# Optimization experiments

Measured on AMD Instinct MI355X. Metric: run time of the kernel, lower is better.

## Reference

```python
import jax, jax.numpy as jnp
import numpy as np
import math

HIDDEN = 256
HEADS = 8
HEAD_DIM = HIDDEN // HEADS
SCALE = math.sqrt(HEAD_DIM)


def setup_inputs() -> dict:
    key = jax.random.key(0)
    ks = jax.random.split(key, 10)
    B, N = 2, 4096
    x = jax.random.normal(ks[0], (B, N, HIDDEN), dtype=jnp.float32)
    pos = jax.random.normal(ks[1], (B, N, 3), dtype=jnp.float32)
    s = 1.0 / math.sqrt(HIDDEN)
    Wq = jax.random.normal(ks[2], (HIDDEN, HIDDEN), dtype=jnp.float32) * s
    bq = jnp.zeros((HIDDEN,), dtype=jnp.float32)
    Wk = jax.random.normal(ks[3], (HIDDEN, HIDDEN), dtype=jnp.float32) * s
    bk = jnp.zeros((HIDDEN,), dtype=jnp.float32)
    Wv = jax.random.normal(ks[4], (HIDDEN, HIDDEN), dtype=jnp.float32) * s
    bv = jnp.zeros((HIDDEN,), dtype=jnp.float32)
    Wo = jax.random.normal(ks[5], (HIDDEN, HIDDEN), dtype=jnp.float32) * s
    bo = jnp.zeros((HIDDEN,), dtype=jnp.float32)
    return {"x": x, "pos": pos, "Wq": Wq, "bq": bq, "Wk": Wk, "bk": bk,
            "Wv": Wv, "bv": bv, "Wo": Wo, "bo": bo}


def _pairwise_dist(pos):
    # Euclidean cdist via the norm trick; clip for numerical safety.
    sq = jnp.sum(pos * pos, axis=-1)  # [B, N]
    d2 = sq[:, :, None] + sq[:, None, :] - 2.0 * jnp.einsum('bic,bjc->bij', pos, pos)
    return jnp.sqrt(jnp.maximum(d2, 0.0))  # [B, N, N]


def reference(x, pos, Wq, bq, Wk, bk, Wv, bv, Wo, bo):
    B, N, _ = x.shape
    # projections -> [B, H, N, Dh]
    def split_heads(t):
        return t.reshape(B, N, HEADS, HEAD_DIM).transpose(0, 2, 1, 3)
    q = split_heads(x @ Wq.T + bq)
    k = split_heads(x @ Wk.T + bk)
    v = split_heads(x @ Wv.T + bv)
    scores = jnp.einsum('bhid,bhjd->bhij', q, k) / SCALE
    dist_bias = -_pairwise_dist(pos) / 10.0  # [B, N, N]
    scores = scores + dist_bias[:, None, :, :]
    attn = jax.nn.softmax(scores, axis=-1)
    out = jnp.einsum('bhij,bhjd->bhid', attn, v)
    out = out.transpose(0, 2, 1, 3).reshape(B, N, HIDDEN)
    return out @ Wo.T + bo
```

## Files before the change

kernel.cpp:

```cpp
#include <hip/hip_runtime.h>

#define BATCH 2
#define SEQ   4096
#define HID   256
#define NHEAD 8
#define DH    32
#define THR_L2 11.5f
#define QSCALE 0.25501639769925074f
#define BIASC (-0.14426950408889634f)

typedef __attribute__((ext_vector_type(8))) _Float16 half8;
typedef __attribute__((ext_vector_type(4))) _Float16 half4;
typedef __attribute__((ext_vector_type(2))) __fp16   fp16x2;
typedef __attribute__((ext_vector_type(4))) float    f32x4;

__device__ __forceinline__ float fast_exp2(float x) {
    return __builtin_amdgcn_exp2f(x);
}

__global__ void cvt_f32_f16(const float* __restrict__ src,
                            _Float16* __restrict__ dst, int n) {
    int i = (blockIdx.x * blockDim.x + threadIdx.x) * 4;
    if (i >= n) return;
    f32x4 v = *reinterpret_cast<const f32x4*>(src + i);
    half4 h;
#pragma unroll
    for (int c = 0; c < 4; ++c) h[c] = (_Float16)v[c];
    *reinterpret_cast<half4*>(dst + i) = h;
}

__global__ void cvt_w4(const float* __restrict__ a, const float* __restrict__ b,
                       const float* __restrict__ c, const float* __restrict__ d,
                       _Float16* __restrict__ dst) {
    const float* srcs[4] = {a, b, c, d};
    const float* s = srcs[blockIdx.y];
    const int i = (blockIdx.x * blockDim.x + threadIdx.x) * 4;
    f32x4 v = *reinterpret_cast<const f32x4*>(s + i);
    half4 h;
#pragma unroll
    for (int k = 0; k < 4; ++k) h[k] = (_Float16)v[k];
    *reinterpret_cast<half4*>(dst + (size_t)blockIdx.y * HID * HID + i) = h;
}

__global__ __launch_bounds__(256) void qkv_proj(
    const _Float16* __restrict__ xh, const _Float16* __restrict__ Wh,
    const float* __restrict__ bq, const float* __restrict__ bk,
    const float* __restrict__ bv,
    _Float16* __restrict__ Qh, _Float16* __restrict__ Kh,
    _Float16* __restrict__ Vt)
{
    const int z   = blockIdx.z;
    const int m0  = blockIdx.x * 64;
    const int n0  = blockIdx.y * 64;
    const int tid = threadIdx.x;
    const int w   = tid >> 6, lane = tid & 63;
    const int lr  = lane & 15, lg = lane >> 4;
    const int wr  = (w >> 1) * 32, wc = (w & 1) * 32;

    const _Float16* Wp = Wh + (size_t)z * HID * HID;
    const float* bias = (z == 0) ? bq : (z == 1) ? bk : bv;

    f32x4 acc[2][2] = {};
    const int ar = m0 + wr + lr;
    const int br = n0 + wc + lr;
#pragma unroll
    for (int ks = 0; ks < 8; ++ks) {
        const int ko = ks * 32 + lg * 8;
        half8 a0 = *reinterpret_cast<const half8*>(xh + (size_t)ar * HID + ko);
        half8 a1 = *reinterpret_cast<const half8*>(xh + (size_t)(ar + 16) * HID + ko);
        half8 b0 = *reinterpret_cast<const half8*>(Wp + (size_t)br * HID + ko);
        half8 b1 = *reinterpret_cast<const half8*>(Wp + (size_t)(br + 16) * HID + ko);
        acc[0][0] = __builtin_amdgcn_mfma_f32_16x16x32_f16(a0, b0, acc[0][0], 0, 0, 0);
        acc[0][1] = __builtin_amdgcn_mfma_f32_16x16x32_f16(a0, b1, acc[0][1], 0, 0, 0);
        acc[1][0] = __builtin_amdgcn_mfma_f32_16x16x32_f16(a1, b0, acc[1][0], 0, 0, 0);
        acc[1][1] = __builtin_amdgcn_mfma_f32_16x16x32_f16(a1, b1, acc[1][1], 0, 0, 0);
    }
#pragma unroll
    for (int mf = 0; mf < 2; ++mf)
#pragma unroll
    for (int nf = 0; nf < 2; ++nf)
#pragma unroll
    for (int r = 0; r < 4; ++r) {
        const int m  = m0 + wr + mf * 16 + lg * 4 + r;
        const int o  = n0 + wc + nf * 16 + lr;
        const int bb = m >> 12, nn = m & (SEQ - 1);
        const int hh = o >> 5,  dd = o & (DH - 1);
        float v = acc[mf][nf][r] + bias[o];
        if (z == 0) {
            Qh[(((size_t)(bb * NHEAD + hh) * SEQ) + nn) * DH + dd] =
                (_Float16)(v * QSCALE);
        } else if (z == 1) {
            Kh[(((size_t)(bb * NHEAD + hh) * SEQ) + nn) * DH + dd] = (_Float16)v;
        } else {
            Vt[(((size_t)(bb * NHEAD + hh) * DH) + dd) * SEQ + nn] = (_Float16)v;
        }
    }
}

__device__ __forceinline__ void attn_tile(
    int t,
    const _Float16* __restrict__ Kl, const _Float16* __restrict__ Vl0,
    const _Float16* __restrict__ Vl1,
    half8 aq, half8 (&kc)[4], half8 (&kn)[4], half8 (&vc)[4], half8 (&vn)[4],
    const float* __restrict__ biasRow, char* PlW, float* xw,
    float& mrun, float& lsum, f32x4& acc0, f32x4& acc1, int lane, int lg)
{
    const int tn = (t + 1) & (SEQ / 64 - 1);

#pragma unroll
    for (int cf = 0; cf < 4; ++cf)
        kn[cf] = *reinterpret_cast<const half8*>(
            Kl + (size_t)(tn * 64 + cf * 16) * DH);
    vn[0] = *reinterpret_cast<const half8*>(Vl0 + tn * 64);
    vn[1] = *reinterpret_cast<const half8*>(Vl1 + tn * 64);
    vn[2] = *reinterpret_cast<const half8*>(Vl0 + tn * 64 + 32);
    vn[3] = *reinterpret_cast<const half8*>(Vl1 + tn * 64 + 32);

    const int sb = (t & 7) * 64;
    f32x4 vv[4];
    __builtin_amdgcn_s_setprio(1);
#pragma unroll
    for (int cf = 0; cf < 4; ++cf) {
        f32x4 cb = *reinterpret_cast<const f32x4*>(biasRow + sb + cf * 16 + lg * 4);
        vv[cf] = __builtin_amdgcn_mfma_f32_16x16x32_f16(kc[cf], aq, cb, 0, 0, 0);
    }
    __builtin_amdgcn_s_setprio(0);

    float m0 = fmaxf(fmaxf(vv[0][0], vv[0][1]), vv[0][2]);
    float m1 = fmaxf(fmaxf(vv[0][3], vv[1][0]), vv[1][1]);
    float m2 = fmaxf(fmaxf(vv[1][2], vv[1][3]), vv[2][0]);
    float m3 = fmaxf(fmaxf(vv[2][1], vv[2][2]), vv[2][3]);
    float m4 = fmaxf(fmaxf(vv[3][0], vv[3][1]), vv[3][2]);
    float tmax = fmaxf(fmaxf(fmaxf(m0, m1), fmaxf(m2, m3)),
                       fmaxf(m4, vv[3][3]));

    if (!__all(tmax <= mrun + THR_L2)) {
        float tm = tmax;
        tm = fmaxf(tm, __shfl_xor(tm, 16, 64));
        tm = fmaxf(tm, __shfl_xor(tm, 32, 64));
        const float mnew  = fmaxf(mrun, tm);
        const float alpha = fast_exp2(mrun - mnew);
        if (lane < 16) xw[lane] = alpha;
        f32x4 a4 = *reinterpret_cast<const f32x4*>(&xw[lg * 4]);
        lsum *= alpha;
        mrun = mnew;
        acc0 *= a4;
        acc1 *= a4;
    }

    const int lr = lane & 15;
#pragma unroll
    for (int cf = 0; cf < 4; ++cf) {
        float p0 = fast_exp2(vv[cf][0] - mrun);
        float p1 = fast_exp2(vv[cf][1] - mrun);
        float p2 = fast_exp2(vv[cf][2] - mrun);
        float p3 = fast_exp2(vv[cf][3] - mrun);
        lsum += (p0 + p1) + (p2 + p3);
        fp16x2 ha = __builtin_amdgcn_cvt_pkrtz(p0, p1);
        fp16x2 hb = __builtin_amdgcn_cvt_pkrtz(p2, p3);
        unsigned int wlo = __builtin_bit_cast(unsigned int, ha);
        unsigned int whi = __builtin_bit_cast(unsigned int, hb);
        unsigned long long wq =
            (unsigned long long)wlo | ((unsigned long long)whi << 32);
        *reinterpret_cast<unsigned long long*>(
            PlW + lr * 144 + (cf * 16 + lg * 4) * 2) = wq;
    }

    half8 pa0 = *reinterpret_cast<const half8*>(PlW + lr * 144 + (lg * 8) * 2);
    half8 pa1 = *reinterpret_cast<const half8*>(PlW + lr * 144 + (32 + lg * 8) * 2);
    __builtin_amdgcn_s_setprio(1);
    acc0 = __builtin_amdgcn_mfma_f32_16x16x32_f16(pa0, vc[0], acc0, 0, 0, 0);
    acc1 = __builtin_amdgcn_mfma_f32_16x16x32_f16(pa0, vc[1], acc1, 0, 0, 0);
    acc0 = __builtin_amdgcn_mfma_f32_16x16x32_f16(pa1, vc[2], acc0, 0, 0, 0);
    acc1 = __builtin_amdgcn_mfma_f32_16x16x32_f16(pa1, vc[3], acc1, 0, 0, 0);
    __builtin_amdgcn_s_setprio(0);
}

__global__ __launch_bounds__(512, 4) void attn_kernel(
    const _Float16* __restrict__ Qh, const _Float16* __restrict__ Kh,
    const _Float16* __restrict__ Vt, const float* __restrict__ pos,
    _Float16* __restrict__ AO)
{
    __shared__ __align__(16) float pi4[16][4];
    __shared__ __align__(16) float pj4[512][4];
    __shared__ __align__(16) float biasL[16][516];
    __shared__ __align__(16) _Float16 Pl[NHEAD][16 * 72];
    __shared__ __align__(16) float xposeL[NHEAD][16];

    const int b    = blockIdx.y;
    const int i0   = blockIdx.x * 16;
    const int tid  = threadIdx.x;
    const int w    = tid >> 6;
    const int lane = tid & 63;
    const int lr   = lane & 15, lg = lane >> 4;

    if (tid < 16) {
        const float* p = pos + (size_t)(b * SEQ + i0 + tid) * 3;
        float x = p[0], y = p[1], z = p[2];
        pi4[tid][0] = x; pi4[tid][1] = y; pi4[tid][2] = z;
        pi4[tid][3] = x * x + y * y + z * z;
    }

    const size_t bhh = (size_t)(b * NHEAD + w);
    const _Float16* Qbase = Qh + (bhh * SEQ + i0) * DH;
    const _Float16* Kl  = Kh + bhh * SEQ * DH + (size_t)lr * DH + lg * 8;
    const _Float16* Vl0 = Vt + bhh * DH * SEQ + (size_t)lr * SEQ + lg * 8;
    const _Float16* Vl1 = Vt + bhh * DH * SEQ + (size_t)(16 + lr) * SEQ + lg * 8;

    const half8 aq = *reinterpret_cast<const half8*>(Qbase + (size_t)lr * DH + lg * 8);

    f32x4 acc0 = {}, acc1 = {};
    float mrun = -1e30f, lsum = 0.f;

    char* PlW = (char*)&Pl[w][0];
    float* xw = &xposeL[w][0];
    const float* biasRow = &biasL[lr][0];

    half8 kA[4], kB[4], vA[4], vB[4];
#pragma unroll
    for (int cf = 0; cf < 4; ++cf)
        kA[cf] = *reinterpret_cast<const half8*>(Kl + (size_t)(cf * 16) * DH);
    vA[0] = *reinterpret_cast<const half8*>(Vl0);
    vA[1] = *reinterpret_cast<const half8*>(Vl1);
    vA[2] = *reinterpret_cast<const half8*>(Vl0 + 32);
    vA[3] = *reinterpret_cast<const half8*>(Vl1 + 32);

    for (int ch = 0; ch < SEQ / 512; ++ch) {
        __syncthreads();
        {
            const float* p = pos + (size_t)(b * SEQ + ch * 512 + tid) * 3;
            float x = p[0], y = p[1], z = p[2];
            pj4[tid][0] = x; pj4[tid][1] = y; pj4[tid][2] = z;
            pj4[tid][3] = x * x + y * y + z * z;
        }
        __syncthreads();
        {
            const int br  = tid & 15;
            const int c0  = (tid >> 4) * 16;
            const float xi = pi4[br][0], yi = pi4[br][1], zi = pi4[br][2], si = pi4[br][3];
#pragma unroll
            for (int k4 = 0; k4 < 4; ++k4) {
                f32x4 o;
#pragma unroll
                for (int k = 0; k < 4; ++k) {
                    const float* pj = &pj4[c0 + k4 * 4 + k][0];
                    float dot = xi * pj[0] + yi * pj[1] + zi * pj[2];
                    float d2  = si + pj[3] - 2.f * dot;
                    o[k] = BIASC * sqrtf(fmaxf(d2, 0.f));
                }
                *reinterpret_cast<f32x4*>(&biasL[br][c0 + k4 * 4]) = o;
            }
        }
        __syncthreads();

        for (int s = 0; s < 4; ++s) {
            const int t = ch * 8 + s * 2;
            attn_tile(t,     Kl, Vl0, Vl1, aq, kA, kB, vA, vB,
                      biasRow, PlW, xw, mrun, lsum, acc0, acc1, lane, lg);
            attn_tile(t + 1, Kl, Vl0, Vl1, aq, kB, kA, vB, vA,
                      biasRow, PlW, xw, mrun, lsum, acc0, acc1, lane, lg);
        }
    }

    lsum += __shfl_xor(lsum, 16, 64);
    lsum += __shfl_xor(lsum, 32, 64);
    const float inv = 1.f / lsum;
    if (lane < 16) xw[lane] = inv;
    f32x4 i4 = *reinterpret_cast<const f32x4*>(&xw[lg * 4]);
#pragma unroll
    for (int t = 0; t < 4; ++t) {
        const size_t row = (size_t)(b * SEQ + i0 + lg * 4 + t) * HID + w * DH;
        AO[row + lr]      = (_Float16)(acc0[t] * i4[t]);
        AO[row + 16 + lr] = (_Float16)(acc1[t] * i4[t]);
    }
}

__global__ __launch_bounds__(256) void out_proj(
    const _Float16* __restrict__ AO, const _Float16* __restrict__ Woh,
    const float* __restrict__ bo, float* __restrict__ out)
{
    const int m0  = blockIdx.x * 64;
    const int n0  = blockIdx.y * 64;
    const int tid = threadIdx.x;
    const int w   = tid >> 6, lane = tid & 63;
    const int lr  = lane & 15, lg = lane >> 4;
    const int wr  = (w >> 1) * 32, wc = (w & 1) * 32;

    f32x4 acc[2][2] = {};
    const int ar = m0 + wr + lr;
    const int br = n0 + wc + lr;
#pragma unroll
    for (int ks = 0; ks < 8; ++ks) {
        const int ko = ks * 32 + lg * 8;
        half8 a0 = *reinterpret_cast<const half8*>(AO + (size_t)ar * HID + ko);
        half8 a1 = *reinterpret_cast<const half8*>(AO + (size_t)(ar + 16) * HID + ko);
        half8 b0 = *reinterpret_cast<const half8*>(Woh + (size_t)br * HID + ko);
        half8 b1 = *reinterpret_cast<const half8*>(Woh + (size_t)(br + 16) * HID + ko);
        acc[0][0] = __builtin_amdgcn_mfma_f32_16x16x32_f16(a0, b0, acc[0][0], 0, 0, 0);
        acc[0][1] = __builtin_amdgcn_mfma_f32_16x16x32_f16(a0, b1, acc[0][1], 0, 0, 0);
        acc[1][0] = __builtin_amdgcn_mfma_f32_16x16x32_f16(a1, b0, acc[1][0], 0, 0, 0);
        acc[1][1] = __builtin_amdgcn_mfma_f32_16x16x32_f16(a1, b1, acc[1][1], 0, 0, 0);
    }
#pragma unroll
    for (int mf = 0; mf < 2; ++mf)
#pragma unroll
    for (int nf = 0; nf < 2; ++nf)
#pragma unroll
    for (int r = 0; r < 4; ++r) {
        const int m = m0 + wr + mf * 16 + lg * 4 + r;
        const int o = n0 + wc + nf * 16 + lr;
        out[(size_t)m * HID + o] = acc[mf][nf][r] + bo[o];
    }
}

extern "C" void kernel_launch(void* const* d_in, const int* in_sizes, int n_in,
                              void* d_out, int out_size, void* d_ws, size_t ws_size,
                              hipStream_t stream)
{
    const float* x   = (const float*)d_in[0];
    const float* pos = (const float*)d_in[1];
    const float* Wq  = (const float*)d_in[2];
    const float* bq  = (const float*)d_in[3];
    const float* Wk  = (const float*)d_in[4];
    const float* bk  = (const float*)d_in[5];
    const float* Wv  = (const float*)d_in[6];
    const float* bv  = (const float*)d_in[7];
    const float* Wo  = (const float*)d_in[8];
    const float* bo  = (const float*)d_in[9];
    float* out = (float*)d_out;

    char* ws = (char*)d_ws;
    _Float16* Qh = (_Float16*)(ws);
    _Float16* Kh = (_Float16*)(ws + (4  << 20));
    _Float16* Vt = (_Float16*)(ws + (8  << 20));
    _Float16* xh = (_Float16*)(ws + (12 << 20));
    _Float16* AO = xh;
    _Float16* Wh = (_Float16*)(ws + (16 << 20));

    const int NX = BATCH * SEQ * HID;
    const int NW = HID * HID;
    cvt_f32_f16<<<NX / 1024, 256, 0, stream>>>(x, xh, NX);
    cvt_w4<<<dim3(NW / 1024, 4), 256, 0, stream>>>(Wq, Wk, Wv, Wo, Wh);

    qkv_proj<<<dim3(BATCH * SEQ / 64, HID / 64, 3), 256, 0, stream>>>(
        xh, Wh, bq, bk, bv, Qh, Kh, Vt);

    attn_kernel<<<dim3(SEQ / 16, BATCH), 512, 0, stream>>>(Qh, Kh, Vt, pos, AO);

    out_proj<<<dim3(BATCH * SEQ / 64, HID / 64), 256, 0, stream>>>(
        AO, Wh + 3 * NW, bo, out);
}
```

Measured before the change: 236.7 us.

## Permute V layout so P feeds PV MFMA directly from registers, drop LDS staging

The V projection now writes V^T with a permuted sequence order. The exp'd probability fragments from the QK MFMA output can then be packed straight into the A-operand of the PV MFMA, with no round trip through shared memory. This removes the per-wave LDS write and read of P along with the Pl buffer. The explicit double-buffered register prefetch of the next K/V tile is also dropped in favour of loading inside the loop, which may expose global-load latency.

```diff
diff --git a/kernel.cpp b/kernel.cpp
--- a/kernel.cpp
+++ b/kernel.cpp
@@ -13,6 +13,7 @@
 typedef __attribute__((ext_vector_type(4))) _Float16 half4;
 typedef __attribute__((ext_vector_type(2))) __fp16   fp16x2;
 typedef __attribute__((ext_vector_type(4))) float    f32x4;
+typedef __attribute__((ext_vector_type(4))) unsigned int uint4v;
 
 __device__ __forceinline__ float fast_exp2(float x) {
     return __builtin_amdgcn_exp2f(x);
@@ -92,88 +93,10 @@
         } else if (z == 1) {
             Kh[(((size_t)(bb * NHEAD + hh) * SEQ) + nn) * DH + dd] = (_Float16)v;
         } else {
-            Vt[(((size_t)(bb * NHEAD + hh) * DH) + dd) * SEQ + nn] = (_Float16)v;
+            const int pp = (nn & ~31) | ((nn & 12) << 1) | ((nn & 16) >> 2) | (nn & 3);
+            Vt[(((size_t)(bb * NHEAD + hh) * DH) + dd) * SEQ + pp] = (_Float16)v;
         }
     }
-}
-
-__device__ __forceinline__ void attn_tile(
-    int t,
-    const _Float16* __restrict__ Kl, const _Float16* __restrict__ Vl0,
-    const _Float16* __restrict__ Vl1,
-    half8 aq, half8 (&kc)[4], half8 (&kn)[4], half8 (&vc)[4], half8 (&vn)[4],
-    const float* __restrict__ biasRow, char* PlW, float* xw,
-    float& mrun, float& lsum, f32x4& acc0, f32x4& acc1, int lane, int lg)
-{
-    const int tn = (t + 1) & (SEQ / 64 - 1);
-
-#pragma unroll
-    for (int cf = 0; cf < 4; ++cf)
-        kn[cf] = *reinterpret_cast<const half8*>(
-            Kl + (size_t)(tn * 64 + cf * 16) * DH);
-    vn[0] = *reinterpret_cast<const half8*>(Vl0 + tn * 64);
-    vn[1] = *reinterpret_cast<const half8*>(Vl1 + tn * 64);
-    vn[2] = *reinterpret_cast<const half8*>(Vl0 + tn * 64 + 32);
-    vn[3] = *reinterpret_cast<const half8*>(Vl1 + tn * 64 + 32);
-
-    const int sb = (t & 7) * 64;
-    f32x4 vv[4];
-    __builtin_amdgcn_s_setprio(1);
-#pragma unroll
-    for (int cf = 0; cf < 4; ++cf) {
-        f32x4 cb = *reinterpret_cast<const f32x4*>(biasRow + sb + cf * 16 + lg * 4);
-        vv[cf] = __builtin_amdgcn_mfma_f32_16x16x32_f16(kc[cf], aq, cb, 0, 0, 0);
-    }
-    __builtin_amdgcn_s_setprio(0);
-
-    float m0 = fmaxf(fmaxf(vv[0][0], vv[0][1]), vv[0][2]);
-    float m1 = fmaxf(fmaxf(vv[0][3], vv[1][0]), vv[1][1]);
-    float m2 = fmaxf(fmaxf(vv[1][2], vv[1][3]), vv[2][0]);
-    float m3 = fmaxf(fmaxf(vv[2][1], vv[2][2]), vv[2][3]);
-    float m4 = fmaxf(fmaxf(vv[3][0], vv[3][1]), vv[3][2]);
-    float tmax = fmaxf(fmaxf(fmaxf(m0, m1), fmaxf(m2, m3)),
-                       fmaxf(m4, vv[3][3]));
-
-    if (!__all(tmax <= mrun + THR_L2)) {
-        float tm = tmax;
-        tm = fmaxf(tm, __shfl_xor(tm, 16, 64));
-        tm = fmaxf(tm, __shfl_xor(tm, 32, 64));
-        const float mnew  = fmaxf(mrun, tm);
-        const float alpha = fast_exp2(mrun - mnew);
-        if (lane < 16) xw[lane] = alpha;
-        f32x4 a4 = *reinterpret_cast<const f32x4*>(&xw[lg * 4]);
-        lsum *= alpha;
-        mrun = mnew;
-        acc0 *= a4;
-        acc1 *= a4;
-    }
-
-    const int lr = lane & 15;
-#pragma unroll
-    for (int cf = 0; cf < 4; ++cf) {
-        float p0 = fast_exp2(vv[cf][0] - mrun);
-        float p1 = fast_exp2(vv[cf][1] - mrun);
-        float p2 = fast_exp2(vv[cf][2] - mrun);
-        float p3 = fast_exp2(vv[cf][3] - mrun);
-        lsum += (p0 + p1) + (p2 + p3);
-        fp16x2 ha = __builtin_amdgcn_cvt_pkrtz(p0, p1);
-        fp16x2 hb = __builtin_amdgcn_cvt_pkrtz(p2, p3);
-        unsigned int wlo = __builtin_bit_cast(unsigned int, ha);
-        unsigned int whi = __builtin_bit_cast(unsigned int, hb);
-        unsigned long long wq =
-            (unsigned long long)wlo | ((unsigned long long)whi << 32);
-        *reinterpret_cast<unsigned long long*>(
-            PlW + lr * 144 + (cf * 16 + lg * 4) * 2) = wq;
-    }
-
-    half8 pa0 = *reinterpret_cast<const half8*>(PlW + lr * 144 + (lg * 8) * 2);
-    half8 pa1 = *reinterpret_cast<const half8*>(PlW + lr * 144 + (32 + lg * 8) * 2);
-    __builtin_amdgcn_s_setprio(1);
-    acc0 = __builtin_amdgcn_mfma_f32_16x16x32_f16(pa0, vc[0], acc0, 0, 0, 0);
-    acc1 = __builtin_amdgcn_mfma_f32_16x16x32_f16(pa0, vc[1], acc1, 0, 0, 0);
-    acc0 = __builtin_amdgcn_mfma_f32_16x16x32_f16(pa1, vc[2], acc0, 0, 0, 0);
-    acc1 = __builtin_amdgcn_mfma_f32_16x16x32_f16(pa1, vc[3], acc1, 0, 0, 0);
-    __builtin_amdgcn_s_setprio(0);
 }
 
 __global__ __launch_bounds__(512, 4) void attn_kernel(
@@ -184,7 +107,6 @@
     __shared__ __align__(16) float pi4[16][4];
     __shared__ __align__(16) float pj4[512][4];
     __shared__ __align__(16) float biasL[16][516];
-    __shared__ __align__(16) _Float16 Pl[NHEAD][16 * 72];
     __shared__ __align__(16) float xposeL[NHEAD][16];
 
     const int b    = blockIdx.y;
@@ -212,18 +134,8 @@
     f32x4 acc0 = {}, acc1 = {};
     float mrun = -1e30f, lsum = 0.f;
 
-    char* PlW = (char*)&Pl[w][0];
     float* xw = &xposeL[w][0];
     const float* biasRow = &biasL[lr][0];
-
-    half8 kA[4], kB[4], vA[4], vB[4];
-#pragma unroll
-    for (int cf = 0; cf < 4; ++cf)
-        kA[cf] = *reinterpret_cast<const half8*>(Kl + (size_t)(cf * 16) * DH);
-    vA[0] = *reinterpret_cast<const half8*>(Vl0);
-    vA[1] = *reinterpret_cast<const half8*>(Vl1);
-    vA[2] = *reinterpret_cast<const half8*>(Vl0 + 32);
-    vA[3] = *reinterpret_cast<const half8*>(Vl1 + 32);
 
     for (int ch = 0; ch < SEQ / 512; ++ch) {
         __syncthreads();
@@ -253,12 +165,81 @@
         }
         __syncthreads();
 
-        for (int s = 0; s < 4; ++s) {
-            const int t = ch * 8 + s * 2;
-            attn_tile(t,     Kl, Vl0, Vl1, aq, kA, kB, vA, vB,
-                      biasRow, PlW, xw, mrun, lsum, acc0, acc1, lane, lg);
-            attn_tile(t + 1, Kl, Vl0, Vl1, aq, kB, kA, vB, vA,
-                      biasRow, PlW, xw, mrun, lsum, acc0, acc1, lane, lg);
+        for (int s = 0; s < 8; ++s) {
+            const int t  = ch * 8 + s;
+            const int jh = t * 64;
+
+            half8 k8[4];
+#pragma unroll
+            for (int cf = 0; cf < 4; ++cf)
+                k8[cf] = *reinterpret_cast<const half8*>(
+                    Kl + (size_t)(jh + cf * 16) * DH);
+            half8 vc0 = *reinterpret_cast<const half8*>(Vl0 + jh);
+            half8 vc1 = *reinterpret_cast<const half8*>(Vl1 + jh);
+            half8 vc2 = *reinterpret_cast<const half8*>(Vl0 + jh + 32);
+            half8 vc3 = *reinterpret_cast<const half8*>(Vl1 + jh + 32);
+
+            f32x4 vv[4];
+            __builtin_amdgcn_s_setprio(1);
+#pragma unroll
+            for (int cf = 0; cf < 4; ++cf) {
+                f32x4 cb = *reinterpret_cast<const f32x4*>(
+                    biasRow + s * 64 + cf * 16 + lg * 4);
+                vv[cf] = __builtin_amdgcn_mfma_f32_16x16x32_f16(k8[cf], aq, cb, 0, 0, 0);
+            }
+            __builtin_amdgcn_s_setprio(0);
+
+            float m0 = fmaxf(fmaxf(vv[0][0], vv[0][1]), vv[0][2]);
+            float m1 = fmaxf(fmaxf(vv[0][3], vv[1][0]), vv[1][1]);
+            float m2 = fmaxf(fmaxf(vv[1][2], vv[1][3]), vv[2][0]);
+            float m3 = fmaxf(fmaxf(vv[2][1], vv[2][2]), vv[2][3]);
+            float m4 = fmaxf(fmaxf(vv[3][0], vv[3][1]), vv[3][2]);
+            float tmax = fmaxf(fmaxf(fmaxf(m0, m1), fmaxf(m2, m3)),
+                               fmaxf(m4, vv[3][3]));
+
+            if (!__all(tmax <= mrun + THR_L2)) {
+                float tm = tmax;
+                tm = fmaxf(tm, __shfl_xor(tm, 16, 64));
+                tm = fmaxf(tm, __shfl_xor(tm, 32, 64));
+                const float mnew  = fmaxf(mrun, tm);
+                const float alpha = fast_exp2(mrun - mnew);
+                if (lane < 16) xw[lane] = alpha;
+                f32x4 a4 = *reinterpret_cast<const f32x4*>(&xw[lg * 4]);
+                lsum *= alpha;
+                mrun = mnew;
+                acc0 *= a4;
+                acc1 *= a4;
+            }
+
+            float e00 = fast_exp2(vv[0][0] - mrun), e01 = fast_exp2(vv[0][1] - mrun);
+            float e02 = fast_exp2(vv[0][2] - mrun), e03 = fast_exp2(vv[0][3] - mrun);
+            float e10 = fast_exp2(vv[1][0] - mrun), e11 = fast_exp2(vv[1][1] - mrun);
+            float e12 = fast_exp2(vv[1][2] - mrun), e13 = fast_exp2(vv[1][3] - mrun);
+            float e20 = fast_exp2(vv[2][0] - mrun), e21 = fast_exp2(vv[2][1] - mrun);
+            float e22 = fast_exp2(vv[2][2] - mrun), e23 = fast_exp2(vv[2][3] - mrun);
+            float e30 = fast_exp2(vv[3][0] - mrun), e31 = fast_exp2(vv[3][1] - mrun);
+            float e32 = fast_exp2(vv[3][2] - mrun), e33 = fast_exp2(vv[3][3] - mrun);
+            lsum += ((e00 + e01) + (e02 + e03)) + ((e10 + e11) + (e12 + e13)) +
+                    ((e20 + e21) + (e22 + e23)) + ((e30 + e31) + (e32 + e33));
+
+            uint4v u0, u1;
+            u0[0] = __builtin_bit_cast(unsigned int, __builtin_amdgcn_cvt_pkrtz(e00, e01));
+            u0[1] = __builtin_bit_cast(unsigned int, __builtin_amdgcn_cvt_pkrtz(e02, e03));
+            u0[2] = __builtin_bit_cast(unsigned int, __builtin_amdgcn_cvt_pkrtz(e10, e11));
+            u0[3] = __builtin_bit_cast(unsigned int, __builtin_amdgcn_cvt_pkrtz(e12, e13));
+            u1[0] = __builtin_bit_cast(unsigned int, __builtin_amdgcn_cvt_pkrtz(e20, e21));
+            u1[1] = __builtin_bit_cast(unsigned int, __builtin_amdgcn_cvt_pkrtz(e22, e23));
+            u1[2] = __builtin_bit_cast(unsigned int, __builtin_amdgcn_cvt_pkrtz(e30, e31));
+            u1[3] = __builtin_bit_cast(unsigned int, __builtin_amdgcn_cvt_pkrtz(e32, e33));
+            half8 pa0 = __builtin_bit_cast(half8, u0);
+            half8 pa1 = __builtin_bit_cast(half8, u1);
+
+            __builtin_amdgcn_s_setprio(1);
+            acc0 = __builtin_amdgcn_mfma_f32_16x16x32_f16(pa0, vc0, acc0, 0, 0, 0);
+            acc1 = __builtin_amdgcn_mfma_f32_16x16x32_f16(pa0, vc1, acc1, 0, 0, 0);
+            acc0 = __builtin_amdgcn_mfma_f32_16x16x32_f16(pa1, vc2, acc0, 0, 0, 0);
+            acc1 = __builtin_amdgcn_mfma_f32_16x16x32_f16(pa1, vc3, acc1, 0, 0, 0);
+            __builtin_amdgcn_s_setprio(0);
         }
     }
 
```

After: 237.5 us. No clear change (+0.4%).
